# Optimization experiments

Measured on AMD Instinct MI355X. Metric: run time of the kernel, lower is better.

Reference implementation:

```python
import jax, jax.numpy as jnp
import numpy as np

N_NODES = 50000
N_EDGES = 800000
N_FEAT = 128
DIM = 128
N_GRAPHS = 512


def setup_inputs() -> dict:
    key = jax.random.key(0)
    k1, k2, k3, k4, k5, k6 = jax.random.split(key, 6)
    x = jax.random.normal(k1, (N_NODES, N_FEAT), dtype=jnp.float32)
    edge_index = jax.random.randint(k2, (2, N_EDGES), 0, N_NODES, dtype=jnp.int64)
    batch = jnp.sort(jax.random.randint(k3, (N_NODES,), 0, N_GRAPHS, dtype=jnp.int64))
    # GCNConv linear weights (bias=False); stored as [in, out] so h = x @ W
    W1 = jax.random.normal(k4, (N_FEAT, DIM), dtype=jnp.float32) * (1.0 / np.sqrt(N_FEAT))
    W2 = jax.random.normal(k5, (DIM, DIM), dtype=jnp.float32) * (1.0 / np.sqrt(DIM))
    Wfc = jax.random.normal(k6, (DIM, 1), dtype=jnp.float32) * (1.0 / np.sqrt(DIM))
    return {"x": x, "edge_index": edge_index, "batch": batch,
            "W1": W1, "W2": W2, "Wfc": Wfc}


def _gcn_conv(x, W, src, dst):
    # PyG GCNConv with normalize=False, bias=False:
    # linear transform, then scatter-add messages from src into dst.
    h = x @ W                                   # [N, dim]
    return jax.ops.segment_sum(h[src], dst, num_segments=N_NODES)


def reference(x, edge_index, batch, W1, W2, Wfc):
    src, dst = edge_index[0], edge_index[1]
    h = jax.nn.relu(_gcn_conv(x, W1, src, dst))  # conv1 + ReLU
    h = _gcn_conv(h, W2, src, dst)               # conv2
    # global_mean_pool over graph ids
    sums = jax.ops.segment_sum(h, batch, num_segments=N_GRAPHS)          # [G, dim]
    counts = jax.ops.segment_sum(jnp.ones((N_NODES,), h.dtype), batch,
                                 num_segments=N_GRAPHS)                   # [G]
    pooled = sums / jnp.maximum(counts, 1.0)[:, None]
    return jax.nn.sigmoid(pooled @ Wfc)          # [G, 1]
```

## Files before the change

### kernel.cpp

```cpp
#include <hip/hip_runtime.h>

#define N_NODES 50000
#define N_EDGES 800000
#define NF 128
#define N_GRAPHS 512
#define STRIDE 64

#define NBINS 391
#define NBLK 196
#define EPB 4096
#define BINCAP 2560

typedef _Float16 f16;
typedef f16 h2    __attribute__((ext_vector_type(2)));
typedef f16 f16x8 __attribute__((ext_vector_type(8)));
typedef float f32x4 __attribute__((ext_vector_type(4)));

union HU { ushort u; _Float16 h; };
__device__ __forceinline__ float h2f(ushort u) { HU x; x.u = u; return (float)x.h; }
__device__ __forceinline__ ushort f2h(float f) { HU x; x.h = (_Float16)f; return x.u; }

union UH2 { uint u; h2 h; };
__device__ __forceinline__ void acc4h(h2* ah, uint4 u) {
  UH2 c;
  c.u = u.x; ah[0] += c.h;
  c.u = u.y; ah[1] += c.h;
  c.u = u.z; ah[2] += c.h;
  c.u = u.w; ah[3] += c.h;
}

__global__ __launch_bounds__(256) void prep(const float* __restrict__ W1,
                                            const float* __restrict__ W2,
                                            const float* __restrict__ Wfc,
                                            ushort* __restrict__ W1T,
                                            float* __restrict__ v,
                                            int* __restrict__ gcur) {
  int b = blockIdx.x;
  if (b < 64) {
    int i = b * 256 + threadIdx.x;
    int n = i >> 7, k = i & 127;
    W1T[i] = f2h(W1[k * 128 + n]);
  } else if (b == 64) {
    if (threadIdx.x < 128) {
      int f = threadIdx.x;
      float s = 0.f;
      for (int j = 0; j < 128; j += 4) {
        float4 w = ((const float4*)(W2 + f * 128))[j >> 2];
        float4 c = ((const float4*)Wfc)[j >> 2];
        s += w.x * c.x + w.y * c.y + w.z * c.z + w.w * c.w;
      }
      v[f] = s;
    }
  } else {
    for (int i = threadIdx.x; i < NBINS; i += 256) gcur[i] = 0;
  }
}

__global__ __launch_bounds__(256) void bin_scatter2(const int* __restrict__ src,
                                                    const int* __restrict__ dst,
                                                    int* __restrict__ gcur,
                                                    uint* __restrict__ ebuf) {
  __shared__ int hist[NBINS];
  __shared__ int base[NBINS];
  for (int i = threadIdx.x; i < NBINS; i += 256) hist[i] = 0;
  __syncthreads();
  int e0 = blockIdx.x * EPB;
  int e1 = e0 + EPB; if (e1 > N_EDGES) e1 = N_EDGES;
  for (int e = e0 + threadIdx.x; e < e1; e += 256)
    atomicAdd(&hist[dst[e] >> 7], 1);
  __syncthreads();
  for (int i = threadIdx.x; i < NBINS; i += 256) {
    int c = hist[i];
    base[i] = (c > 0) ? atomicAdd(&gcur[i], c) : 0;
    hist[i] = 0;
  }
  __syncthreads();
  for (int e = e0 + threadIdx.x; e < e1; e += 256) {
    int d = dst[e];
    int b = d >> 7;
    int loc = atomicAdd(&hist[b], 1);
    ebuf[(size_t)b * BINCAP + base[b] + loc] = ((uint)d << 16) | (uint)src[e];
  }
}

__global__ __launch_bounds__(256) void csr_from_bins(const uint* __restrict__ ebuf,
                                                     const int* __restrict__ gcur,
                                                     int* __restrict__ deg,
                                                     ushort* __restrict__ col16) {
  __shared__ int dl[128];
  const int bin = blockIdx.x;
  const int n0 = bin << 7;
  if (threadIdx.x < 128) dl[threadIdx.x] = 0;
  __syncthreads();
  int cnt_e = gcur[bin];
  int j0 = bin * BINCAP;
  for (int j = j0 + threadIdx.x; j < j0 + cnt_e; j += 256) {
    uint e = ebuf[j];
    int d = (int)(e >> 16);
    int slot = atomicAdd(&dl[d - n0], 1);
    col16[(size_t)d * STRIDE + slot] = (ushort)(e & 0xFFFFu);
  }
  __syncthreads();
  int cnt = N_NODES - n0; if (cnt > 128) cnt = 128;
  if (threadIdx.x < cnt) deg[n0 + threadIdx.x] = dl[threadIdx.x];
}

__global__ __launch_bounds__(256) void gemm_mfma(const float* __restrict__ x,
                                                 const ushort* __restrict__ W1T,
                                                 ushort* __restrict__ y16, int M) {
  __shared__ ushort ly[4][16][136];
  const int tid = threadIdx.x;
  const int w = tid >> 6, l = tid & 63;
  const int row0 = blockIdx.x * 64 + w * 16;
  const int mrow = l & 15, kg = l >> 4;
  const int row = row0 + mrow;

  f32x4 acc[8] = {};
  for (int kc = 0; kc < 4; ++kc) {
    const int cb = kc * 32 + kg * 8;
    f16x8 af = {};
    if (row < M) {
      float4 xlo = *(const float4*)(x + (size_t)row * 128 + cb);
      float4 xhi = *(const float4*)(x + (size_t)row * 128 + cb + 4);
      af[0] = (f16)xlo.x; af[1] = (f16)xlo.y; af[2] = (f16)xlo.z; af[3] = (f16)xlo.w;
      af[4] = (f16)xhi.x; af[5] = (f16)xhi.y; af[6] = (f16)xhi.z; af[7] = (f16)xhi.w;
    }
#pragma unroll
    for (int nt = 0; nt < 8; ++nt) {
      uint4 wb = *(const uint4*)(W1T + ((nt * 16 + mrow) << 7) + cb);
      f16x8 bf = *(const f16x8*)&wb;
      acc[nt] = __builtin_amdgcn_mfma_f32_16x16x32_f16(af, bf, acc[nt], 0, 0, 0);
    }
  }
#pragma unroll
  for (int nt = 0; nt < 8; ++nt)
#pragma unroll
    for (int r = 0; r < 4; ++r)
      ly[w][kg * 4 + r][nt * 16 + mrow] = f2h(acc[nt][r]);
  __syncthreads();
#pragma unroll
  for (int t = 0; t < 8; ++t) {
    int idx = t * 64 + l;
    int r2 = idx >> 5, c2 = idx & 31;
    int gr = row0 + r2;
    if (gr < M)
      ((uint2*)y16)[(size_t)gr * 32 + c2] = *(const uint2*)&ly[w][r2][c2 * 4];
  }
}

__global__ __launch_bounds__(256) void gather_qdot(const ushort* __restrict__ y16,
                                                   const int* __restrict__ deg,
                                                   const ushort* __restrict__ col16,
                                                   const float* __restrict__ vq,
                                                   float* __restrict__ q) {
  int n = (blockIdx.x * 256 + threadIdx.x) >> 6;
  if (n >= N_NODES) return;
  const int lane = threadIdx.x & 63;
  const int eg = lane >> 4;
  const int fl = lane & 15;

  int dg = deg[n];
  const ushort* cp = col16 + (size_t)n * STRIDE;
  h2 ah[4] = {};

  int j = eg;
  for (; j + 12 < dg; j += 16) {
    int s0 = cp[j], s1 = cp[j + 4], s2 = cp[j + 8], s3 = cp[j + 12];
    uint4 a = ((const uint4*)y16)[(size_t)s0 * 16 + fl];
    uint4 b = ((const uint4*)y16)[(size_t)s1 * 16 + fl];
    uint4 c = ((const uint4*)y16)[(size_t)s2 * 16 + fl];
    uint4 d = ((const uint4*)y16)[(size_t)s3 * 16 + fl];
    acc4h(ah, a);
    acc4h(ah, b);
    acc4h(ah, c);
    acc4h(ah, d);
  }
  for (; j + 4 < dg; j += 8) {
    int s0 = cp[j], s1 = cp[j + 4];
    uint4 a = ((const uint4*)y16)[(size_t)s0 * 16 + fl];
    uint4 b = ((const uint4*)y16)[(size_t)s1 * 16 + fl];
    acc4h(ah, a);
    acc4h(ah, b);
  }
  if (j < dg) {
    uint4 a = ((const uint4*)y16)[(size_t)cp[j] * 16 + fl];
    acc4h(ah, a);
  }

#pragma unroll
  for (int k = 0; k < 4; ++k) {
    UH2 c, t;
    c.h = ah[k];
    t.u = (uint)__shfl_xor((int)c.u, 16, 64); ah[k] += t.h;
    c.h = ah[k];
    t.u = (uint)__shfl_xor((int)c.u, 32, 64); ah[k] += t.h;
  }
  float4 v0 = ((const float4*)vq)[fl * 2];
  float4 v1 = ((const float4*)vq)[fl * 2 + 1];
  float p = fmaxf((float)ah[0].x, 0.f) * v0.x + fmaxf((float)ah[0].y, 0.f) * v0.y +
            fmaxf((float)ah[1].x, 0.f) * v0.z + fmaxf((float)ah[1].y, 0.f) * v0.w +
            fmaxf((float)ah[2].x, 0.f) * v1.x + fmaxf((float)ah[2].y, 0.f) * v1.y +
            fmaxf((float)ah[3].x, 0.f) * v1.z + fmaxf((float)ah[3].y, 0.f) * v1.w;
  p += __shfl_xor(p, 1, 64);
  p += __shfl_xor(p, 2, 64);
  p += __shfl_xor(p, 4, 64);
  p += __shfl_xor(p, 8, 64);
  if (lane == 0) q[n] = p;
}

__global__ __launch_bounds__(256) void pool_q(const float* __restrict__ q,
                                              const int* __restrict__ deg,
                                              const ushort* __restrict__ col16,
                                              const int* __restrict__ batch,
                                              float* __restrict__ out) {
  __shared__ float red[4];
  int g = blockIdx.x, tid = threadIdx.x;

  int lo = 0, hi = N_NODES;
  while (lo < hi) { int m = (lo + hi) >> 1; if (batch[m] < g) lo = m + 1; else hi = m; }
  int s0 = lo;
  lo = 0; hi = N_NODES;
  while (lo < hi) { int m = (lo + hi) >> 1; if (batch[m] <= g) lo = m + 1; else hi = m; }
  int s1 = lo;

  float sum = 0.f;
  for (int n = s0 + (tid >> 3); n < s1; n += 32) {
    int dg = deg[n];
    const ushort* cp = col16 + (size_t)n * STRIDE;
    for (int j = tid & 7; j < dg; j += 8) sum += q[cp[j]];
  }
#pragma unroll
  for (int off = 32; off > 0; off >>= 1) sum += __shfl_down(sum, off, 64);
  if ((tid & 63) == 0) red[tid >> 6] = sum;
  __syncthreads();
  if (tid == 0) {
    float z = red[0] + red[1] + red[2] + red[3];
    float cnt = fmaxf((float)(s1 - s0), 1.0f);
    z /= cnt;
    out[g] = 1.0f / (1.0f + expf(-z));
  }
}

extern "C" void kernel_launch(void* const* d_in, const int* in_sizes, int n_in,
                              void* d_out, int out_size, void* d_ws, size_t ws_size,
                              hipStream_t stream) {
  const float* x   = (const float*)d_in[0];
  const int*   ei  = (const int*)d_in[1];
  const int*   src = ei;
  const int*   dst = ei + N_EDGES;
  const int* batch = (const int*)d_in[2];
  const float* W1  = (const float*)d_in[3];
  const float* W2  = (const float*)d_in[4];
  const float* Wfc = (const float*)d_in[5];
  float* out = (float*)d_out;

  ushort* y16  = (ushort*)d_ws;
  ushort* col16 = y16 + (size_t)N_NODES * NF;
  int* deg     = (int*)(col16 + (size_t)N_NODES * STRIDE);
  float* q     = (float*)(deg + N_NODES);
  float* v     = q + N_NODES;
  ushort* W1T  = (ushort*)(v + NF + 32);
  int* gcur    = (int*)(W1T + 16384 + 64);
  uint* ebuf   = (uint*)(gcur + NBINS + 32);

  const int gemm_grid = (N_NODES + 63) / 64;
  const int gath_grid = (N_NODES * 64 + 255) / 256;

  prep<<<66, 256, 0, stream>>>(W1, W2, Wfc, W1T, v, gcur);

  bin_scatter2<<<NBLK, 256, 0, stream>>>(src, dst, gcur, ebuf);
  csr_from_bins<<<NBINS, 256, 0, stream>>>(ebuf, gcur, deg, col16);

  gemm_mfma<<<gemm_grid, 256, 0, stream>>>(x, W1T, y16, N_NODES);

  gather_qdot<<<gath_grid, 256, 0, stream>>>(y16, deg, col16, v, q);

  pool_q<<<N_GRAPHS, 256, 0, stream>>>(q, deg, col16, batch, out);
}
```

Measured before the change: 96.16 us.

## Fuse edge binning with GEMM launch and batch gather loads

Merges the edge-binning pass and the MFMA GEMM into one launch. Block ranges pick which job they run, and the binning blocks reuse the GEMM's shared-memory tile for their histograms. The two independent phases can then overlap and one launch is saved. The gather loop also issues up to eight neighbour row loads before accumulating them, which raises memory-level parallelism, with a scalar tail for degrees above 32. The cost is higher register pressure and a shared-memory footprint sized for the larger of the two roles.

```diff
diff --git a/kernel.cpp b/kernel.cpp
--- a/kernel.cpp
+++ b/kernel.cpp
@@ -56,62 +56,42 @@
   }
 }
 
-__global__ __launch_bounds__(256) void bin_scatter2(const int* __restrict__ src,
-                                                    const int* __restrict__ dst,
-                                                    int* __restrict__ gcur,
-                                                    uint* __restrict__ ebuf) {
-  __shared__ int hist[NBINS];
-  __shared__ int base[NBINS];
-  for (int i = threadIdx.x; i < NBINS; i += 256) hist[i] = 0;
-  __syncthreads();
-  int e0 = blockIdx.x * EPB;
-  int e1 = e0 + EPB; if (e1 > N_EDGES) e1 = N_EDGES;
-  for (int e = e0 + threadIdx.x; e < e1; e += 256)
-    atomicAdd(&hist[dst[e] >> 7], 1);
-  __syncthreads();
-  for (int i = threadIdx.x; i < NBINS; i += 256) {
-    int c = hist[i];
-    base[i] = (c > 0) ? atomicAdd(&gcur[i], c) : 0;
-    hist[i] = 0;
-  }
-  __syncthreads();
-  for (int e = e0 + threadIdx.x; e < e1; e += 256) {
-    int d = dst[e];
-    int b = d >> 7;
-    int loc = atomicAdd(&hist[b], 1);
-    ebuf[(size_t)b * BINCAP + base[b] + loc] = ((uint)d << 16) | (uint)src[e];
-  }
-}
-
-__global__ __launch_bounds__(256) void csr_from_bins(const uint* __restrict__ ebuf,
-                                                     const int* __restrict__ gcur,
-                                                     int* __restrict__ deg,
-                                                     ushort* __restrict__ col16) {
-  __shared__ int dl[128];
-  const int bin = blockIdx.x;
-  const int n0 = bin << 7;
-  if (threadIdx.x < 128) dl[threadIdx.x] = 0;
-  __syncthreads();
-  int cnt_e = gcur[bin];
-  int j0 = bin * BINCAP;
-  for (int j = j0 + threadIdx.x; j < j0 + cnt_e; j += 256) {
-    uint e = ebuf[j];
-    int d = (int)(e >> 16);
-    int slot = atomicAdd(&dl[d - n0], 1);
-    col16[(size_t)d * STRIDE + slot] = (ushort)(e & 0xFFFFu);
-  }
-  __syncthreads();
-  int cnt = N_NODES - n0; if (cnt > 128) cnt = 128;
-  if (threadIdx.x < cnt) deg[n0 + threadIdx.x] = dl[threadIdx.x];
-}
-
-__global__ __launch_bounds__(256) void gemm_mfma(const float* __restrict__ x,
-                                                 const ushort* __restrict__ W1T,
-                                                 ushort* __restrict__ y16, int M) {
+__global__ __launch_bounds__(256) void fused_bin_gemm(
+    const int* __restrict__ src, const int* __restrict__ dst,
+    int* __restrict__ gcur, uint* __restrict__ ebuf,
+    const float* __restrict__ x, const ushort* __restrict__ W1T,
+    ushort* __restrict__ y16, int M) {
   __shared__ ushort ly[4][16][136];
+
+  if (blockIdx.x < NBLK) {
+    int* hist = (int*)&ly[0][0][0];
+    int* base = hist + NBINS;
+    for (int i = threadIdx.x; i < NBINS; i += 256) hist[i] = 0;
+    __syncthreads();
+    int e0 = blockIdx.x * EPB;
+    int e1 = e0 + EPB; if (e1 > N_EDGES) e1 = N_EDGES;
+    for (int e = e0 + threadIdx.x; e < e1; e += 256)
+      atomicAdd(&hist[dst[e] >> 7], 1);
+    __syncthreads();
+    for (int i = threadIdx.x; i < NBINS; i += 256) {
+      int c = hist[i];
+      base[i] = (c > 0) ? atomicAdd(&gcur[i], c) : 0;
+      hist[i] = 0;
+    }
+    __syncthreads();
+    for (int e = e0 + threadIdx.x; e < e1; e += 256) {
+      int d = dst[e];
+      int b = d >> 7;
+      int loc = atomicAdd(&hist[b], 1);
+      ebuf[(size_t)b * BINCAP + base[b] + loc] = ((uint)d << 16) | (uint)src[e];
+    }
+    return;
+  }
+
+  const int bid = blockIdx.x - NBLK;
   const int tid = threadIdx.x;
   const int w = tid >> 6, l = tid & 63;
-  const int row0 = blockIdx.x * 64 + w * 16;
+  const int row0 = bid * 64 + w * 16;
   const int mrow = l & 15, kg = l >> 4;
   const int row = row0 + mrow;
 
@@ -146,6 +126,28 @@
     if (gr < M)
       ((uint2*)y16)[(size_t)gr * 32 + c2] = *(const uint2*)&ly[w][r2][c2 * 4];
   }
+}
+
+__global__ __launch_bounds__(256) void csr_from_bins(const uint* __restrict__ ebuf,
+                                                     const int* __restrict__ gcur,
+                                                     int* __restrict__ deg,
+                                                     ushort* __restrict__ col16) {
+  __shared__ int dl[128];
+  const int bin = blockIdx.x;
+  const int n0 = bin << 7;
+  if (threadIdx.x < 128) dl[threadIdx.x] = 0;
+  __syncthreads();
+  int cnt_e = gcur[bin];
+  int j0 = bin * BINCAP;
+  for (int j = j0 + threadIdx.x; j < j0 + cnt_e; j += 256) {
+    uint e = ebuf[j];
+    int d = (int)(e >> 16);
+    int slot = atomicAdd(&dl[d - n0], 1);
+    col16[(size_t)d * STRIDE + slot] = (ushort)(e & 0xFFFFu);
+  }
+  __syncthreads();
+  int cnt = N_NODES - n0; if (cnt > 128) cnt = 128;
+  if (threadIdx.x < cnt) deg[n0 + threadIdx.x] = dl[threadIdx.x];
 }
 
 __global__ __launch_bounds__(256) void gather_qdot(const ushort* __restrict__ y16,
@@ -163,26 +165,18 @@
   const ushort* cp = col16 + (size_t)n * STRIDE;
   h2 ah[4] = {};
 
-  int j = eg;
-  for (; j + 12 < dg; j += 16) {
-    int s0 = cp[j], s1 = cp[j + 4], s2 = cp[j + 8], s3 = cp[j + 12];
-    uint4 a = ((const uint4*)y16)[(size_t)s0 * 16 + fl];
-    uint4 b = ((const uint4*)y16)[(size_t)s1 * 16 + fl];
-    uint4 c = ((const uint4*)y16)[(size_t)s2 * 16 + fl];
-    uint4 d = ((const uint4*)y16)[(size_t)s3 * 16 + fl];
-    acc4h(ah, a);
-    acc4h(ah, b);
-    acc4h(ah, c);
-    acc4h(ah, d);
-  }
-  for (; j + 4 < dg; j += 8) {
-    int s0 = cp[j], s1 = cp[j + 4];
-    uint4 a = ((const uint4*)y16)[(size_t)s0 * 16 + fl];
-    uint4 b = ((const uint4*)y16)[(size_t)s1 * 16 + fl];
-    acc4h(ah, a);
-    acc4h(ah, b);
-  }
-  if (j < dg) {
+  uint4 u[8];
+#pragma unroll
+  for (int k = 0; k < 8; ++k) {
+    int j = eg + k * 4;
+    if (j < dg) u[k] = ((const uint4*)y16)[(size_t)cp[j] * 16 + fl];
+  }
+#pragma unroll
+  for (int k = 0; k < 8; ++k) {
+    int j = eg + k * 4;
+    if (j < dg) acc4h(ah, u[k]);
+  }
+  for (int j = eg + 32; j < dg; j += 4) {
     uint4 a = ((const uint4*)y16)[(size_t)cp[j] * 16 + fl];
     acc4h(ah, a);
   }
@@ -268,11 +262,11 @@
 
   prep<<<66, 256, 0, stream>>>(W1, W2, Wfc, W1T, v, gcur);
 
-  bin_scatter2<<<NBLK, 256, 0, stream>>>(src, dst, gcur, ebuf);
+  fused_bin_gemm<<<NBLK + gemm_grid, 256, 0, stream>>>(src, dst, gcur, ebuf,
+                                                       x, W1T, y16, N_NODES);
+
   csr_from_bins<<<NBINS, 256, 0, stream>>>(ebuf, gcur, deg, col16);
 
-  gemm_mfma<<<gemm_grid, 256, 0, stream>>>(x, W1T, y16, N_NODES);
-
   gather_qdot<<<gath_grid, 256, 0, stream>>>(y16, deg, col16, v, q);
 
   pool_q<<<N_GRAPHS, 256, 0, stream>>>(q, deg, col16, batch, out);
```

Measured after the change: 86.88 us (median of 2 runs). -9.7%, faster.
